# Performance work log

Measured on AMD Instinct MI355X. Metric: run time of the kernel, lower is better.

The kernel has to match this reference:

```python
import jax, jax.numpy as jnp
import numpy as np

NBINS = (128, 64, 32)   # knots per stacked transform
N_GENES = 5000
N_ELEM = 4_000_000


def _split_parameters(unnormalized):
    # mirror of QuadraticSplineStack._split_parameters: [heights(n), widths(n-1)] per transform
    splits = []
    for n in NBINS:
        splits += [n, n - 1]
    parts = jnp.split(unnormalized, np.cumsum(splits)[:-1].tolist(), axis=-1)
    return list(zip(parts[0::2], parts[1::2]))


def _bin_search(table, gix, x):
    # vectorized per-element binary search: searchsorted(table[gix], x, side='right') - 1,
    # clamped to valid bin range [0, K-2]. table: [G, K] sorted; gix, x: [N].
    K = table.shape[-1]
    lo = jnp.zeros(x.shape, jnp.int32)
    hi = jnp.full(x.shape, K, jnp.int32)
    for _ in range(int(np.ceil(np.log2(K + 1)))):
        mid = jnp.clip((lo + hi) // 2, 0, K - 1)
        pred = table[gix, mid] <= x
        lo = jnp.where(pred, mid + 1, lo)
        hi = jnp.where(pred, hi, mid)
    return jnp.clip(lo - 1, 0, K - 2)


def _quadratic_spline_forward(x, gix, unnorm_heights, unnorm_widths):
    # per-gene tables
    widths = jax.nn.softmax(unnorm_widths, axis=-1)                      # [G, n-1]
    locs = jnp.cumsum(widths, axis=-1)
    locs = jnp.pad(locs.at[:, -1].set(1.0), ((0, 0), (1, 0)))            # [G, n] bin_locations
    eh = jnp.exp(unnorm_heights)                                         # [G, n]
    area = jnp.sum(0.5 * (eh[:, :-1] + eh[:, 1:]) * widths, axis=-1, keepdims=True)
    heights = eh / area                                                  # pdf knot heights, integrates to 1
    cdf = jnp.cumsum(0.5 * (heights[:, :-1] + heights[:, 1:]) * widths, axis=-1)
    left_cdf = jnp.pad(cdf.at[:, -1].set(1.0), ((0, 0), (1, 0)))         # [G, n] bin_left_cdf

    # locate bin per element, then gather scalar coefficients
    b = _bin_search(locs, gix, x)                                        # [N] in [0, n-2]
    w = widths[gix, b]
    lh = heights[gix, b]
    rh = heights[gix, b + 1]
    bl = locs[gix, b]
    lc = left_cdf[gix, b]

    alpha = (x - bl) / w
    out = (0.5 * (rh - lh) * w) * alpha * alpha + (lh * w) * alpha + lc
    out = jnp.clip(out, 0.0, 1.0)
    logabsdet = jnp.log(alpha * (rh - lh) + lh)
    return out, logabsdet


def setup_inputs() -> dict:
    key = jax.random.key(0)
    k1, k2, k3 = jax.random.split(key, 3)
    x = jax.random.uniform(k1, (N_ELEM,), dtype=jnp.float32, minval=1e-4, maxval=1.0 - 1e-4)
    local_gene_ix = jax.random.randint(k2, (N_ELEM,), 0, N_GENES)
    total = sum(n + (n - 1) for n in NBINS)  # 445
    unnormalized = jax.random.normal(k3, (N_GENES, total), dtype=jnp.float32) * 0.1
    return {"x": x, "local_gene_ix": local_gene_ix, "unnormalized": unnormalized}


def reference(x, local_gene_ix, unnormalized):
    gix = local_gene_ix.astype(jnp.int32)
    outputs = x
    logabsdet = jnp.zeros_like(x)
    for uh, uw in _split_parameters(unnormalized):
        outputs, lad = _quadratic_spline_forward(outputs, gix, uh, uw)
        logabsdet = logabsdet + lad
    return outputs, logabsdet
```

## Files before the change

kernel.cpp:

```cpp
#include <hip/hip_runtime.h>
#include <hip/hip_bf16.h>
#include <hip/hip_fp16.h>

#define N_GENES_MAX 5000
#define N_ELEM_MAX  4000000
#define PARAMS_PER_GENE 445

__device__ uint2 g_k0[(size_t)N_GENES_MAX * 128];
__device__ uint2 g_k1[(size_t)N_GENES_MAX * 64];
__device__ uint2 g_k2[(size_t)N_GENES_MAX * 32];
__device__ uint2 g_mid[N_ELEM_MAX];

static __device__ __forceinline__ unsigned f2h(float f) {
    union { __half h; unsigned short u; } c;
    c.h = __float2half_rn(f);
    return (unsigned)c.u;
}
static __device__ __forceinline__ float h2f(unsigned u) {
    union { unsigned short u; __half h; } c;
    c.u = (unsigned short)u;
    return __half2float(c.h);
}

static __device__ __forceinline__ float wscan_incl(float v) {
    const int lane = threadIdx.x & 63;
    #pragma unroll
    for (int off = 1; off < 64; off <<= 1) {
        float u = __shfl_up(v, off, 64);
        if (lane >= off) v += u;
    }
    return v;
}
static __device__ __forceinline__ float wmax64(float v) {
    #pragma unroll
    for (int off = 32; off > 0; off >>= 1) v = fmaxf(v, __shfl_xor(v, off, 64));
    return v;
}
static __device__ __forceinline__ float wsum64(float v) {
    #pragma unroll
    for (int off = 32; off > 0; off >>= 1) v += __shfl_xor(v, off, 64);
    return v;
}

__global__ void build_knots(const float* __restrict__ params) {
    const int g = blockIdx.x;
    const int t = blockIdx.y;
    const int ns[3]   = {128, 64, 32};
    const int poff[3] = {0, 255, 382};

    const int n = ns[t];
    const int m = n - 1;
    const float* ph = params + (size_t)g * PARAMS_PER_GENE + poff[t];
    const float* pw = ph + n;

    __shared__ float s2[2];
    __shared__ float s_scan[128];
    __shared__ float s_h[129];
    __shared__ float s_loc[128];
    __shared__ float s_cdf[128];

    const int tid  = threadIdx.x;
    const int lane = tid & 63;
    const int wv   = tid >> 6;

    const float uw = (tid < m) ? pw[tid] : -1e30f;
    float vmax = wmax64(uw);
    if (lane == 0) s2[wv] = vmax;
    __syncthreads();
    const float mx = fmaxf(s2[0], s2[1]);
    __syncthreads();

    const float e = (tid < m) ? __expf(uw - mx) : 0.0f;

    float sc = wscan_incl(e);
    if (lane == 63) s2[wv] = sc;
    __syncthreads();
    if (wv == 1) sc += s2[0];
    s_scan[tid] = sc;
    __syncthreads();

    const float S = s_scan[m - 1];
    const float invS = 1.0f / S;
    if (tid == 0) s_loc[0] = 0.0f;
    if (tid < m) s_loc[tid + 1] = (tid == m - 1) ? 1.0f : s_scan[tid] * invS;
    const float w_i = e * invS;

    const float eh = (tid < n) ? __expf(ph[tid]) : 0.0f;
    s_h[tid] = eh;
    if (tid == 0) s_h[128] = 0.0f;
    __syncthreads();

    const float term = (tid < m) ? 0.5f * (s_h[tid] + s_h[tid + 1]) * w_i : 0.0f;
    float ts = wsum64(term);
    if (lane == 0) s2[wv] = ts;
    __syncthreads();
    const float area = s2[0] + s2[1];
    __syncthreads();

    const float ia = 1.0f / area;
    const float hgt = eh * ia;

    float c = wscan_incl(term * ia);
    if (lane == 63) s2[wv] = c;
    __syncthreads();
    if (wv == 1) c += s2[0];
    s_scan[tid] = c;
    __syncthreads();

    if (tid == 0) s_cdf[0] = 0.0f;
    if (tid < m) s_cdf[tid + 1] = (tid == m - 1) ? 1.0f : s_scan[tid];
    __syncthreads();

    if (tid < n) {
        const float loc = s_loc[tid];
        uint2 kt;
        kt.x = __float_as_uint(loc);
        kt.y = (f2h(hgt) << 16) | f2h(s_cdf[tid] - loc);
        if (t == 0)      g_k0[(size_t)g * 128 + tid] = kt;
        else if (t == 1) g_k1[(size_t)g * 64 + tid] = kt;
        else             g_k2[(size_t)g * 32 + tid] = kt;
    }
}

template <int K>
static __device__ __forceinline__ void stage(const uint2* __restrict__ kn,
                                             float& x, float& lad) {
    int b = (int)(x * (float)(K - 1));
    b = (b < 0) ? 0 : ((b > K - 2) ? K - 2 : b);
    uint2 k0 = kn[b];
    uint2 k1 = kn[b + 1];
    float l0 = __uint_as_float(k0.x);
    float l1 = __uint_as_float(k1.x);
    while (b > 0 && l0 > x) {
        --b;
        k1 = k0; l1 = l0;
        k0 = kn[b]; l0 = __uint_as_float(k0.x);
    }
    while (b < K - 2 && l1 <= x) {
        ++b;
        k0 = k1; l0 = l1;
        k1 = kn[b + 1]; l1 = __uint_as_float(k1.x);
    }
    const float lh = h2f(k0.y >> 16);
    const float rh = h2f(k1.y >> 16);
    const float lc = l0 + h2f(k0.y & 0xffffu);
    const float w  = l1 - l0;
    const float alpha = (x - l0) / w;
    float o = (0.5f * (rh - lh) * w) * alpha * alpha + (lh * w) * alpha + lc;
    o = fminf(fmaxf(o, 0.0f), 1.0f);
    lad += __logf(alpha * (rh - lh) + lh);
    x = o;
}

typedef float fvec2 __attribute__((ext_vector_type(2)));
typedef int   ivec2 __attribute__((ext_vector_type(2)));
typedef unsigned uvec4 __attribute__((ext_vector_type(4)));

__global__ void spline_evalA(const float* __restrict__ x_in,
                             const int* __restrict__ gix, int N) {
    const int i = blockIdx.x * blockDim.x + threadIdx.x;
    const int i2 = i * 2;
    if (i2 + 1 < N) {
        const fvec2 xv = __builtin_nontemporal_load((const fvec2*)(x_in + i2));
        const ivec2 gv = __builtin_nontemporal_load((const ivec2*)(gix + i2));
        float x0 = xv.x, x1 = xv.y;
        float l0 = 0.0f, l1 = 0.0f;
        stage<128>(g_k0 + (size_t)gv.x * 128, x0, l0);
        stage<128>(g_k0 + (size_t)gv.y * 128, x1, l1);
        uvec4 mid;
        mid.x = __float_as_uint(x0);
        mid.y = ((unsigned)gv.x << 16) | f2h(l0);
        mid.z = __float_as_uint(x1);
        mid.w = ((unsigned)gv.y << 16) | f2h(l1);
        __builtin_nontemporal_store(mid, (uvec4*)(g_mid + i2));
    } else if (i2 < N) {
        float x0 = x_in[i2];
        float l0 = 0.0f;
        const int g = gix[i2];
        stage<128>(g_k0 + (size_t)g * 128, x0, l0);
        uint2 m;
        m.x = __float_as_uint(x0);
        m.y = ((unsigned)g << 16) | f2h(l0);
        g_mid[i2] = m;
    }
}

__global__ void spline_evalB(float* __restrict__ out, int N) {
    const int i = blockIdx.x * blockDim.x + threadIdx.x;
    const int i2 = i * 2;
    if (i2 + 1 < N) {
        const uvec4 mid = __builtin_nontemporal_load((const uvec4*)(g_mid + i2));
        float x0 = __uint_as_float(mid.x);
        float x1 = __uint_as_float(mid.z);
        const int g0 = (int)(mid.y >> 16);
        const int g1 = (int)(mid.w >> 16);
        float l0 = h2f(mid.y & 0xffffu);
        float l1 = h2f(mid.w & 0xffffu);
        stage<64>(g_k1 + (size_t)g0 * 64, x0, l0);
        stage<64>(g_k1 + (size_t)g1 * 64, x1, l1);
        stage<32>(g_k2 + (size_t)g0 * 32, x0, l0);
        stage<32>(g_k2 + (size_t)g1 * 32, x1, l1);
        fvec2 o0; o0.x = x0; o0.y = x1;
        fvec2 o1; o1.x = l0; o1.y = l1;
        __builtin_nontemporal_store(o0, (fvec2*)(out + i2));
        __builtin_nontemporal_store(o1, (fvec2*)(out + N + i2));
    } else if (i2 < N) {
        const uint2 mid = g_mid[i2];
        float x0 = __uint_as_float(mid.x);
        const int g0 = (int)(mid.y >> 16);
        float l0 = h2f(mid.y & 0xffffu);
        stage<64>(g_k1 + (size_t)g0 * 64, x0, l0);
        stage<32>(g_k2 + (size_t)g0 * 32, x0, l0);
        out[i2] = x0;
        out[N + i2] = l0;
    }
}

extern "C" void kernel_launch(void* const* d_in, const int* in_sizes, int n_in,
                              void* d_out, int out_size, void* d_ws, size_t ws_size,
                              hipStream_t stream) {
    const float* x      = (const float*)d_in[0];
    const int*   gix    = (const int*)d_in[1];
    const float* params = (const float*)d_in[2];
    float* out = (float*)d_out;

    const int N = in_sizes[0];
    const int G = in_sizes[2] / PARAMS_PER_GENE;

    build_knots<<<dim3(G, 3), 128, 0, stream>>>(params);

    const int block = 256;
    const int nh = (N + 1) / 2;
    const int grid = (nh + block - 1) / block;
    spline_evalA<<<grid, block, 0, stream>>>(x, gix, N);
    spline_evalB<<<grid, block, 0, stream>>>(out, N);
}
```

Before: 189.7 us.

## Counting-sort elements by gene before a fused three-stage spline evaluation

Adds a histogram, a prefix scan and an atomic scatter that group elements by gene index into packed records. Each record holds x quantised to 16 bits, the gene id and the original element index. A single fused eval kernel then runs all three spline stages from one combined per-gene knot table, remaps blocks across the XCDs and scatters results back to their original positions. The aim is to improve cache locality of the per-gene table lookups and to drop the intermediate write and read between the two previous eval kernels. In exchange it adds two passes of global atomics over a few thousand counters, uncoalesced output writes, and precision loss from quantising the input x.

```diff
diff --git a/kernel.cpp b/kernel.cpp
--- a/kernel.cpp
+++ b/kernel.cpp
@@ -6,10 +6,10 @@
 #define N_ELEM_MAX  4000000
 #define PARAMS_PER_GENE 445
 
-__device__ uint2 g_k0[(size_t)N_GENES_MAX * 128];
-__device__ uint2 g_k1[(size_t)N_GENES_MAX * 64];
-__device__ uint2 g_k2[(size_t)N_GENES_MAX * 32];
-__device__ uint2 g_mid[N_ELEM_MAX];
+__device__ uint2 g_tab[(size_t)N_GENES_MAX * 224];
+__device__ uint2 g_srec[N_ELEM_MAX];
+__device__ unsigned g_hist[N_GENES_MAX];
+__device__ unsigned g_cursor[N_GENES_MAX];
 
 static __device__ __forceinline__ unsigned f2h(float f) {
     union { __half h; unsigned short u; } c;
@@ -27,6 +27,15 @@
     #pragma unroll
     for (int off = 1; off < 64; off <<= 1) {
         float u = __shfl_up(v, off, 64);
+        if (lane >= off) v += u;
+    }
+    return v;
+}
+static __device__ __forceinline__ int wscan_incl_i(int v) {
+    const int lane = threadIdx.x & 63;
+    #pragma unroll
+    for (int off = 1; off < 64; off <<= 1) {
+        int u = __shfl_up(v, off, 64);
         if (lane >= off) v += u;
     }
     return v;
@@ -47,6 +56,9 @@
     const int t = blockIdx.y;
     const int ns[3]   = {128, 64, 32};
     const int poff[3] = {0, 255, 382};
+    const int koff[3] = {0, 128, 192};
+
+    if (t == 0 && threadIdx.x == 0) g_hist[g] = 0;
 
     const int n = ns[t];
     const int m = n - 1;
@@ -116,9 +128,82 @@
         uint2 kt;
         kt.x = __float_as_uint(loc);
         kt.y = (f2h(hgt) << 16) | f2h(s_cdf[tid] - loc);
-        if (t == 0)      g_k0[(size_t)g * 128 + tid] = kt;
-        else if (t == 1) g_k1[(size_t)g * 64 + tid] = kt;
-        else             g_k2[(size_t)g * 32 + tid] = kt;
+        g_tab[(size_t)g * 224 + koff[t] + tid] = kt;
+    }
+}
+
+typedef float fvec4 __attribute__((ext_vector_type(4)));
+typedef int   ivec4 __attribute__((ext_vector_type(4)));
+typedef unsigned uvec4 __attribute__((ext_vector_type(4)));
+
+__global__ void hist_kernel(const int* __restrict__ gix, int N) {
+    const int i4 = (blockIdx.x * blockDim.x + threadIdx.x) * 4;
+    if (i4 + 3 < N) {
+        const ivec4 gv = *(const ivec4*)(gix + i4);
+        atomicAdd(&g_hist[gv.x], 1u);
+        atomicAdd(&g_hist[gv.y], 1u);
+        atomicAdd(&g_hist[gv.z], 1u);
+        atomicAdd(&g_hist[gv.w], 1u);
+    } else {
+        for (int j = i4; j < N; ++j) atomicAdd(&g_hist[gix[j]], 1u);
+    }
+}
+
+__global__ void scan_kernel(int G) {
+    const int t = threadIdx.x;
+    const int lane = t & 63;
+    const int wv = t >> 6;
+    __shared__ int ws[16];
+
+    int c[5];
+    int s = 0;
+    #pragma unroll
+    for (int j = 0; j < 5; ++j) {
+        const int idx = t * 5 + j;
+        const int v = (idx < G) ? (int)g_hist[idx] : 0;
+        c[j] = s;
+        s += v;
+    }
+    int sc = wscan_incl_i(s);
+    if (lane == 63) ws[wv] = sc;
+    __syncthreads();
+    int wbase = 0;
+    for (int k = 0; k < wv; ++k) wbase += ws[k];
+    const int excl = wbase + sc - s;
+    #pragma unroll
+    for (int j = 0; j < 5; ++j) {
+        const int idx = t * 5 + j;
+        if (idx < G) g_cursor[idx] = (unsigned)(excl + c[j]);
+    }
+}
+
+__global__ void scatter_kernel(const float* __restrict__ x_in,
+                               const int* __restrict__ gix, int N) {
+    const int i4 = (blockIdx.x * blockDim.x + threadIdx.x) * 4;
+    if (i4 + 3 < N) {
+        const fvec4 xv = __builtin_nontemporal_load((const fvec4*)(x_in + i4));
+        const ivec4 gv = __builtin_nontemporal_load((const ivec4*)(gix + i4));
+        #pragma unroll
+        for (int k = 0; k < 4; ++k) {
+            const int g = (k == 0) ? gv.x : (k == 1) ? gv.y : (k == 2) ? gv.z : gv.w;
+            const float xf = (k == 0) ? xv.x : (k == 1) ? xv.y : (k == 2) ? xv.z : xv.w;
+            const unsigned pos = atomicAdd(&g_cursor[g], 1u);
+            const unsigned xq = __float2uint_rn(fminf(fmaxf(xf, 0.0f), 1.0f) * 65535.0f);
+            uint2 r;
+            r.x = xq | ((unsigned)g << 16);
+            r.y = (unsigned)(i4 + k);
+            g_srec[pos] = r;
+        }
+    } else {
+        for (int j = i4; j < N; ++j) {
+            const int g = gix[j];
+            const unsigned pos = atomicAdd(&g_cursor[g], 1u);
+            const unsigned xq = __float2uint_rn(fminf(fmaxf(x_in[j], 0.0f), 1.0f) * 65535.0f);
+            uint2 r;
+            r.x = xq | ((unsigned)g << 16);
+            r.y = (unsigned)j;
+            g_srec[pos] = r;
+        }
     }
 }
 
@@ -152,67 +237,46 @@
     x = o;
 }
 
-typedef float fvec2 __attribute__((ext_vector_type(2)));
-typedef int   ivec2 __attribute__((ext_vector_type(2)));
-typedef unsigned uvec4 __attribute__((ext_vector_type(4)));
-
-__global__ void spline_evalA(const float* __restrict__ x_in,
-                             const int* __restrict__ gix, int N) {
-    const int i = blockIdx.x * blockDim.x + threadIdx.x;
-    const int i2 = i * 2;
+__global__ void eval_kernel(float* __restrict__ out, int N, int nwg) {
+    const int o = blockIdx.x;
+    const int xcd = o & 7;
+    const int pos = o >> 3;
+    const int q = nwg >> 3;
+    const int r = nwg & 7;
+    const int bid = (xcd < r ? xcd * (q + 1) : r * (q + 1) + (xcd - r) * q) + pos;
+
+    const int i = bid * blockDim.x + threadIdx.x;
+    const long i2 = (long)i * 2;
     if (i2 + 1 < N) {
-        const fvec2 xv = __builtin_nontemporal_load((const fvec2*)(x_in + i2));
-        const ivec2 gv = __builtin_nontemporal_load((const ivec2*)(gix + i2));
-        float x0 = xv.x, x1 = xv.y;
+        const uvec4 rr = __builtin_nontemporal_load((const uvec4*)(g_srec + i2));
+        float x0 = (float)(rr.x & 0xffffu) * (1.0f / 65535.0f);
+        float x1 = (float)(rr.z & 0xffffu) * (1.0f / 65535.0f);
+        const int g0 = (int)(rr.x >> 16);
+        const int g1 = (int)(rr.z >> 16);
         float l0 = 0.0f, l1 = 0.0f;
-        stage<128>(g_k0 + (size_t)gv.x * 128, x0, l0);
-        stage<128>(g_k0 + (size_t)gv.y * 128, x1, l1);
-        uvec4 mid;
-        mid.x = __float_as_uint(x0);
-        mid.y = ((unsigned)gv.x << 16) | f2h(l0);
-        mid.z = __float_as_uint(x1);
-        mid.w = ((unsigned)gv.y << 16) | f2h(l1);
-        __builtin_nontemporal_store(mid, (uvec4*)(g_mid + i2));
+        const uint2* t0 = g_tab + (size_t)g0 * 224;
+        const uint2* t1 = g_tab + (size_t)g1 * 224;
+        stage<128>(t0, x0, l0);
+        stage<128>(t1, x1, l1);
+        stage<64>(t0 + 128, x0, l0);
+        stage<64>(t1 + 128, x1, l1);
+        stage<32>(t0 + 192, x0, l0);
+        stage<32>(t1 + 192, x1, l1);
+        out[rr.y] = x0;
+        out[(size_t)N + rr.y] = l0;
+        out[rr.w] = x1;
+        out[(size_t)N + rr.w] = l1;
     } else if (i2 < N) {
-        float x0 = x_in[i2];
+        const uint2 rr = g_srec[i2];
+        float x0 = (float)(rr.x & 0xffffu) * (1.0f / 65535.0f);
+        const int g0 = (int)(rr.x >> 16);
         float l0 = 0.0f;
-        const int g = gix[i2];
-        stage<128>(g_k0 + (size_t)g * 128, x0, l0);
-        uint2 m;
-        m.x = __float_as_uint(x0);
-        m.y = ((unsigned)g << 16) | f2h(l0);
-        g_mid[i2] = m;
-    }
-}
-
-__global__ void spline_evalB(float* __restrict__ out, int N) {
-    const int i = blockIdx.x * blockDim.x + threadIdx.x;
-    const int i2 = i * 2;
-    if (i2 + 1 < N) {
-        const uvec4 mid = __builtin_nontemporal_load((const uvec4*)(g_mid + i2));
-        float x0 = __uint_as_float(mid.x);
-        float x1 = __uint_as_float(mid.z);
-        const int g0 = (int)(mid.y >> 16);
-        const int g1 = (int)(mid.w >> 16);
-        float l0 = h2f(mid.y & 0xffffu);
-        float l1 = h2f(mid.w & 0xffffu);
-        stage<64>(g_k1 + (size_t)g0 * 64, x0, l0);
-        stage<64>(g_k1 + (size_t)g1 * 64, x1, l1);
-        stage<32>(g_k2 + (size_t)g0 * 32, x0, l0);
-        stage<32>(g_k2 + (size_t)g1 * 32, x1, l1);
-        fvec2 o0; o0.x = x0; o0.y = x1;
-        fvec2 o1; o1.x = l0; o1.y = l1;
-        __builtin_nontemporal_store(o0, (fvec2*)(out + i2));
-        __builtin_nontemporal_store(o1, (fvec2*)(out + N + i2));
-    } else if (i2 < N) {
-        const uint2 mid = g_mid[i2];
-        float x0 = __uint_as_float(mid.x);
-        const int g0 = (int)(mid.y >> 16);
-        float l0 = h2f(mid.y & 0xffffu);
-        stage<64>(g_k1 + (size_t)g0 * 64, x0, l0);
-        stage<32>(g_k2 + (size_t)g0 * 32, x0, l0);
-        out[i2] = x0;
-        out[N + i2] = l0;
+        const uint2* t0 = g_tab + (size_t)g0 * 224;
+        stage<128>(t0, x0, l0);
+        stage<64>(t0 + 128, x0, l0);
+        stage<32>(t0 + 192, x0, l0);
+        out[rr.y] = x0;
+        out[(size_t)N + rr.y] = l0;
     }
 }
 
@@ -230,8 +294,11 @@
     build_knots<<<dim3(G, 3), 128, 0, stream>>>(params);
 
     const int block = 256;
+    const int n4 = (N + 3) / 4;
+    hist_kernel<<<(n4 + block - 1) / block, block, 0, stream>>>(gix, N);
+    scan_kernel<<<1, 1024, 0, stream>>>(G);
+    scatter_kernel<<<(n4 + block - 1) / block, block, 0, stream>>>(x, gix, N);
     const int nh = (N + 1) / 2;
-    const int grid = (nh + block - 1) / block;
-    spline_evalA<<<grid, block, 0, stream>>>(x, gix, N);
-    spline_evalB<<<grid, block, 0, stream>>>(out, N);
-}
+    const int nwg = (nh + block - 1) / block;
+    eval_kernel<<<nwg, block, 0, stream>>>(out, N, nwg);
+}
```

Result: slower. 653.2 us (+244.3%).
